# Kernel tuning notes

Measured on AMD Instinct MI355X. Metric: run time of the kernel, lower is better.

The kernel has to match this reference:

```python
import jax, jax.numpy as jnp
import numpy as np

EPS = float(np.finfo(float).eps)
NUM_RFS = 1

def conv3d(x, w):
    # x: [N,C,D,H,W], w: [O,I,kd,kh,kw], VALID, stride 1 (matches F.conv3d defaults)
    return jax.lax.conv_general_dilated(
        x, w, window_strides=(1, 1, 1), padding='VALID',
        dimension_numbers=('NCDHW', 'OIDHW', 'NCDHW'))

def setup_inputs() -> dict:
    key = jax.random.key(0)
    k1, k2, k3, k4 = jax.random.split(key, 4)
    x = jax.random.normal(k1, (1, 1, 3, 394, 394), jnp.float32)
    x_prev = jax.random.normal(k2, (1, 1, 3, 394, 394), jnp.float32)
    # params stored post-permute as [out_ch, in_ch, kt, kh, kw]
    filts_temp = jax.random.normal(k3, (16, 1, 3, 11, 11), jnp.float32)
    filts_notemp = jax.random.normal(k4, (16, 1, 1, 11, 11), jnp.float32)
    return {"x": x, "x_prev": x_prev, "filts_temp": filts_temp, "filts_notemp": filts_notemp}

def reference(x, x_prev, filts_temp, filts_notemp):
    corr_x = NUM_RFS * filts_temp.shape[3]  # kh
    corr_y = NUM_RFS * filts_temp.shape[4]  # kw
    num_filts = filts_temp.shape[0] + filts_notemp.shape[0]

    def feats(v):
        vt = jax.nn.relu(conv3d(v, filts_temp)) / 2           # [1,16,1,H',W'] (T==kt)
        vn = jax.nn.relu(conv3d(v[:, :, -1:, :, :], filts_notemp))  # last frame, [1,16,1,H',W']
        return jnp.concatenate([vt, vn], axis=1)              # [1,32,1,H',W']

    f = feats(x)
    fp = feats(x_prev)
    # channel-wise normalization
    x1 = f / (jnp.sum(f, axis=1, keepdims=True) + EPS)
    x1_prev = fp / (jnp.sum(fp, axis=1, keepdims=True) + EPS)

    y_max, x_max = x1.shape[3], x1.shape[4]
    yc = y_max - 2 * corr_y
    xc = x_max - 2 * corr_x
    # cropped current-frame channels become conv filters: [nf,1,1,yc,xc]
    x1_filts = x1[:, :, :, corr_y:y_max - corr_y, corr_x:x_max - corr_x].reshape(
        num_filts, 1, 1, yc, xc)
    prev = x1_prev.reshape(1, 1, num_filts, y_max, x_max)
    # normalized cross-correlation via conv3d: out [1, nf, nf, 2cy+1, 2cx+1]
    x2 = conv3d(prev, x1_filts)
    x2 = x2.reshape(1, num_filts, num_filts, 2 * corr_y + 1, 2 * corr_x + 1)
    x2 = x2 / ((y_max - 2 * corr_y) * (x_max - 2 * corr_y))  # faithful to original (uses corr_y twice)
    return x1, x2
```

## Files before the change

### kernel.cpp

```cpp
#include <hip/hip_runtime.h>
#include <hip/hip_bf16.h>


typedef unsigned short ushort_t;
typedef unsigned int uint_t;
typedef unsigned char uchar_t;
typedef __attribute__((ext_vector_type(4))) float f32x4;
typedef __attribute__((ext_vector_type(16))) float f32x16;
typedef __attribute__((ext_vector_type(4))) uint_t uint4_t;
typedef __attribute__((ext_vector_type(2))) uint_t uint2_t;

#define EPSF 2.2204460492503131e-16f
#define X1_N (32*384*384)
#define X2_N (32*32*23*23)

#define FILTB_BYTES (372*48*32*8)
#define PREVB_STRIDE 432
#define PREVB_BYTES (32*385*PREVB_STRIDE)
#define ZERO_BYTES ((size_t)FILTB_BYTES + PREVB_BYTES)
#define FT2_ELEMS (16*45*12)

#define YMAX 367
#define NCHUNKS 16
#define INV_AREA (1.0f/131044.0f)

#define SB_COPY_B 432
#define SB_DYB_B  (8*SB_COPY_B)
#define SB_ROW_B  (4*SB_DYB_B)

__device__ __forceinline__ uint_t f32_to_e4m3(float f) {
  if (f < 0.015625f)
    return (uint_t)__float2int_rn(f * 512.0f);
  uint_t b = __builtin_bit_cast(uint_t, f);
  int e = (int)(b >> 23) - 127;
  uint_t m = b & 0x7FFFFFu;
  uint_t keep = m >> 20;
  uint_t rest = m & 0xFFFFFu;
  keep += (rest > 0x80000u) || (rest == 0x80000u && (keep & 1u));
  if (keep == 8u) { keep = 0u; e += 1; }
  if (e > 8) return 0x7Eu;
  return (uint_t)(((e + 7) << 3) | keep);
}

__global__ void prep_kernel(const float* __restrict__ ft, const float* __restrict__ fn,
                            float* __restrict__ fT2)
{
  const int e = blockIdx.x * 256 + threadIdx.x;
  if (e < FT2_ELEMS) {
    const int chp = e / 540;
    const int rem = e - chp * 540;
    const int row = rem / 12;
    const int j = rem - row * 12;
    float v = 0.f;
    if (j < 11) {
      if (row < 33)      v = ft[chp * 363 + row * 11 + j];
      else if (row < 44) v = fn[chp * 121 + (row - 33) * 11 + j];
    }
    fT2[e] = v;
  }
}

__global__ __launch_bounds__(128, 4) void feat_kernel(
    const float* __restrict__ xcur, const float* __restrict__ xprev,
    const float* __restrict__ fT2,
    float* __restrict__ out_x1, uchar_t* __restrict__ prevb)
{
  __shared__ float sPx[3 * 18 * 28];
  const int tid = threadIdx.x;
  const int chp = tid & 15;
  const int r = tid >> 4;
  const int j0 = blockIdx.x * 16;
  const int i0 = blockIdx.y * 8;
  const int i = i0 + r;
  const int mode = blockIdx.z;
  const float* __restrict__ xin = mode ? xprev : xcur;

  for (int e = tid; e < 3 * 18 * 26; e += 128) {
    const int t = e / 468;
    const int rem = e - t * 468;
    const int ri = rem / 26;
    const int ci = rem - ri * 26;
    sPx[(t * 18 + ri) * 28 + ci] = xin[((size_t)t * 394 + i0 + ri) * 394 + j0 + ci];
  }
  __syncthreads();

  const float* __restrict__ fbase = fT2 + chp * 540;

  float accT[16], accN[16];
#pragma unroll
  for (int p = 0; p < 16; ++p) { accT[p] = 0.f; accN[p] = 0.f; }

#pragma unroll
  for (int t = 0; t < 3; ++t) {
    for (int a = 0; a < 11; ++a) {
      const float* row = &sPx[(t * 18 + r + a) * 28];
      float wv[26];
#pragma unroll
      for (int k = 0; k < 6; ++k) {
        const f32x4 q = *(const f32x4*)(row + 4 * k);
        wv[4 * k + 0] = q[0]; wv[4 * k + 1] = q[1];
        wv[4 * k + 2] = q[2]; wv[4 * k + 3] = q[3];
      }
      wv[24] = row[24]; wv[25] = row[25];

      const float* fr = fbase + (t * 11 + a) * 12;
      const f32x4 fq0 = *(const f32x4*)(fr);
      const f32x4 fq1 = *(const f32x4*)(fr + 4);
      const f32x4 fq2 = *(const f32x4*)(fr + 8);
      float fv[12];
#pragma unroll
      for (int k = 0; k < 4; ++k) { fv[k] = fq0[k]; fv[4+k] = fq1[k]; fv[8+k] = fq2[k]; }
      float fv2[12];
      if (t == 2) {
        const float* fr2 = fbase + (33 + a) * 12;
        const f32x4 g0 = *(const f32x4*)(fr2);
        const f32x4 g1 = *(const f32x4*)(fr2 + 4);
        const f32x4 g2 = *(const f32x4*)(fr2 + 8);
#pragma unroll
        for (int k = 0; k < 4; ++k) { fv2[k] = g0[k]; fv2[4+k] = g1[k]; fv2[8+k] = g2[k]; }
      }

#pragma unroll
      for (int b = 0; b < 11; ++b) {
        const float fT = fv[b];
#pragma unroll
        for (int p = 0; p < 16; ++p) accT[p] = fmaf(wv[b + p], fT, accT[p]);
        if (t == 2) {
          const float fN = fv2[b];
#pragma unroll
          for (int p = 0; p < 16; ++p) accN[p] = fmaf(wv[b + p], fN, accN[p]);
        }
      }
    }
  }

  float o0[16], o1[16];
#pragma unroll
  for (int p = 0; p < 16; ++p) {
    const float vT = fmaxf(accT[p], 0.f) * 0.5f;
    const float vN = fmaxf(accN[p], 0.f);
    float s = vT + vN;
    s += __shfl_xor(s, 1);  s += __shfl_xor(s, 2);
    s += __shfl_xor(s, 4);  s += __shfl_xor(s, 8);
    const float inv = 1.f / (s + EPSF);
    o0[p] = vT * inv;
    o1[p] = vN * inv;
  }

  if (mode == 0) {
#pragma unroll
    for (int q = 0; q < 4; ++q) {
      f32x4 v0 = {o0[4*q], o0[4*q+1], o0[4*q+2], o0[4*q+3]};
      f32x4 v1 = {o1[4*q], o1[4*q+1], o1[4*q+2], o1[4*q+3]};
      *(f32x4*)(out_x1 + (size_t)chp * 147456 + i * 384 + j0 + 4 * q) = v0;
      *(f32x4*)(out_x1 + (size_t)(chp + 16) * 147456 + i * 384 + j0 + 4 * q) = v1;
    }
  } else {
    uint4_t u0, u1;
#pragma unroll
    for (int q = 0; q < 4; ++q) {
      u0[q] = f32_to_e4m3(o0[4*q]) | (f32_to_e4m3(o0[4*q+1]) << 8) |
              (f32_to_e4m3(o0[4*q+2]) << 16) | (f32_to_e4m3(o0[4*q+3]) << 24);
      u1[q] = f32_to_e4m3(o1[4*q]) | (f32_to_e4m3(o1[4*q+1]) << 8) |
              (f32_to_e4m3(o1[4*q+2]) << 16) | (f32_to_e4m3(o1[4*q+3]) << 24);
    }
    *(uint4_t*)(prevb + ((size_t)chp * 385 + i) * PREVB_STRIDE + j0) = u0;
    *(uint4_t*)(prevb + ((size_t)(chp + 16) * 385 + i) * PREVB_STRIDE + j0) = u1;
  }
}

__global__ __launch_bounds__(256) void pack_kernel(
    const float* __restrict__ x1, uchar_t* __restrict__ filtb)
{
  const int e = blockIdx.x * 256 + threadIdx.x;
  if (e >= 362 * 46 * 32) return;
  const int o = e & 31;
  const int q = e >> 5;
  const int xb = q % 46;
  const int rowr = q / 46 + 5;
  const int i = rowr + 6;
  const int j0 = 11 + xb * 8;
  const float* src = x1 + (size_t)o * 147456 + i * 384 + j0;
  uint_t w0 = 0, w1 = 0;
#pragma unroll
  for (int k = 0; k < 4; ++k) {
    w0 |= f32_to_e4m3((j0 + k     <= 372) ? src[k]     : 0.f) << (8 * k);
    w1 |= f32_to_e4m3((j0 + 4 + k <= 372) ? src[4 + k] : 0.f) << (8 * k);
  }
  uint2_t u = {w0, w1};
  *(uint2_t*)(filtb + (((size_t)(rowr * 48 + xb) * 32 + o) << 3)) = u;
}

__global__ __launch_bounds__(768, 3) void corr_kernel(
    const uchar_t* __restrict__ filtb, const uchar_t* __restrict__ prevb,
    float* __restrict__ x2)
{
  __shared__ uint_t sB[2 * 2 * (SB_ROW_B / 4)];

  const int tid = threadIdx.x;
  const int lane = tid & 63;
  const int wv = tid >> 6;
  const int cg = (wv >= 6) ? 1 : 0;
  const int w = wv - 6 * cg;
  const int kg = lane >> 5;
  const int nn = lane & 31;

  const int chpair = blockIdx.x / NCHUNKS;
  const int chunk = blockIdx.x % NCHUNKS;
  const int ch = 2 * chpair + cg;
  const int y0 = (chunk * YMAX) / NCHUNKS;
  const int y1 = ((chunk + 1) * YMAX) / NCHUNKS;

  uint_t* const sBg = sB + cg * (2 * (SB_ROW_B / 4));

  int boffB[3];
#pragma unroll
  for (int nt = 0; nt < 3; ++nt) {
    const int n = nt * 32 + nn;
    const int dyb = n / 24;
    const int dxr = n - 24 * dyb;
    const int dx = (dxr < 23) ? dxr : 22;
    const int s = dx & 7;
    boffB[nt] = dyb * SB_DYB_B + s * SB_COPY_B + (dx >> 3) * 8 + kg * 8;
  }

  const int tl = tid - cg * 384;
  const bool st_act = (tl < 104);
  const int sdyb = st_act ? (tl / 26) : 0;
  const int sg = tl - 26 * (st_act ? (tl / 26) : 0);
  const uchar_t* srcbase = prevb + ((size_t)(ch * 385 + 6 * sdyb)) * PREVB_STRIDE;
  const int dstoff = sdyb * (SB_DYB_B / 4) + 4 * sg;

  uint_t st0 = 0, st1 = 0, st2 = 0, st3 = 0, st4 = 0, st5 = 0;

  auto load_st = [&](int yy) {
    const uint_t* sw = (const uint_t*)(srcbase + (size_t)yy * PREVB_STRIDE) + 4 * sg;
    const uint4_t lo = *(const uint4_t*)(sw);
    const uint2_t hi = *(const uint2_t*)(sw + 4);
    st0 = lo.x; st1 = lo.y; st2 = lo.z; st3 = lo.w; st4 = hi.x; st5 = hi.y;
  };

  auto write_shift = [&](int buf) {
    uint_t* dst = sBg + buf * (SB_ROW_B / 4) + dstoff;
    const uint_t wd[6] = {st0, st1, st2, st3, st4, st5};
#pragma unroll
    for (int s = 0; s < 8; ++s) {
      const int off = s >> 2;
      const int b = (s & 3) * 8;
      uint4_t v;
      if (b == 0) {
        v = uint4_t{wd[off], wd[off + 1], wd[off + 2], wd[off + 3]};
      } else {
        v = uint4_t{(wd[off]     >> b) | (wd[off + 1] << (32 - b)),
                    (wd[off + 1] >> b) | (wd[off + 2] << (32 - b)),
                    (wd[off + 2] >> b) | (wd[off + 3] << (32 - b)),
                    (wd[off + 3] >> b) | (wd[off + 4] << (32 - b))};
      }
      *(uint4_t*)(dst + s * (SB_COPY_B / 4)) = v;
    }
  };

  f32x16 acc[3];
#pragma unroll
  for (int nt = 0; nt < 3; ++nt)
#pragma unroll
    for (int r = 0; r < 16; ++r) acc[nt][r] = 0.f;

  if (st_act) {
    load_st(y0);
    write_shift(0);
    if (y0 + 1 < y1) load_st(y0 + 1);
  }

  const uchar_t* aptr = filtb + (size_t)(y0 - w + 5) * 12288 + kg * 256 + nn * 8;
  long Af0 = *(const long*)(aptr);
  long Af1 = *(const long*)(aptr + 512);

  __syncthreads();

  for (int y = y0; y < y1; ++y) {
    const int pb = (y - y0) & 1;

    if (st_act && y + 1 < y1) write_shift(pb ^ 1);
    if (st_act && y + 2 < y1) load_st(y + 2);

    const char* sBrd = (const char*)sBg + pb * SB_ROW_B;

    long Af2, Bf[3], Bfn[3];
#pragma unroll
    for (int nt = 0; nt < 3; ++nt)
      Bf[nt] = *(const long*)(sBrd + boffB[nt]);

#pragma unroll
    for (int Kt = 0; Kt < 24; ++Kt) {
      Af2 = *(const long*)(aptr + ((Kt + 2) << 9));
      const int Ktb = (Kt + 1 < 24) ? Kt + 1 : 23;
#pragma unroll
      for (int nt = 0; nt < 3; ++nt)
        Bfn[nt] = *(const long*)(sBrd + boffB[nt] + (Ktb << 4));
#pragma unroll
      for (int nt = 0; nt < 3; ++nt)
        acc[nt] = __builtin_amdgcn_mfma_f32_32x32x16_fp8_fp8(
            Af0, Bf[nt], acc[nt], 0, 0, 0);
      Af0 = Af1; Af1 = Af2;
#pragma unroll
      for (int nt = 0; nt < 3; ++nt) Bf[nt] = Bfn[nt];
    }
    aptr += 12288;

    __syncthreads();
  }

#pragma unroll
  for (int nt = 0; nt < 3; ++nt) {
    const int n = nt * 32 + nn;
    const int dyb = n / 24;
    const int dxr = n - 24 * dyb;
    if (dxr < 23) {
      const int dy = w + 6 * dyb;
      if (dy <= 22) {
#pragma unroll
        for (int r = 0; r < 16; ++r) {
          const int o = (r & 3) + 8 * (r >> 2) + 4 * kg;
          atomicAdd(&x2[((o * 32 + ch) * 23 + dy) * 23 + dxr],
                    acc[nt][r] * INV_AREA);
        }
      }
    }
  }
}

extern "C" void kernel_launch(void* const* d_in, const int* in_sizes, int n_in,
                              void* d_out, int out_size, void* d_ws, size_t ws_size,
                              hipStream_t stream)
{
  const float* x     = (const float*)d_in[0];
  const float* xprev = (const float*)d_in[1];
  const float* ft    = (const float*)d_in[2];
  const float* fn    = (const float*)d_in[3];
  float* out = (float*)d_out;

  uchar_t* filtb = (uchar_t*)d_ws;
  uchar_t* prevb = filtb + FILTB_BYTES;
  float* fT2 = (float*)(prevb + PREVB_BYTES);

  hipMemsetAsync(d_ws, 0, ZERO_BYTES, stream);
  hipMemsetAsync(out + X1_N, 0, (size_t)X2_N * sizeof(float), stream);

  prep_kernel<<<dim3((FT2_ELEMS + 255) / 256), 256, 0, stream>>>(ft, fn, fT2);
  feat_kernel<<<dim3(24, 48, 2), 128, 0, stream>>>(x, xprev, fT2, out, prevb);
  pack_kernel<<<dim3((362 * 46 * 32 + 255) / 256), 256, 0, stream>>>(out, filtb);
  corr_kernel<<<dim3(16 * NCHUNKS), 768, 0, stream>>>(filtb, prevb, out + X1_N);
}
```

Baseline: 303.4 us.

## Stage filter rows through an LDS ring buffer in the correlation kernel

The correlation kernel now keeps the fp8 filter (A operand) rows in an 8-row LDS ring buffer instead of reading them directly from global memory in the inner MFMA loop. Each block loads one new row per iteration with a 16-byte-per-thread cooperative load, then stores it to LDS after the MFMA loop. The 12 waves share that row instead of each re-fetching its own global loads. The cost is about 98 KB more shared memory through dynamic allocation, which may reduce occupancy. A-fragment reads also become LDS reads that compete with the B-operand LDS traffic.

New measurement: 293.7 us. -3.2%, faster.

```diff
diff --git a/kernel.cpp b/kernel.cpp
--- a/kernel.cpp
+++ b/kernel.cpp
@@ -14,6 +14,7 @@
 #define X1_N (32*384*384)
 #define X2_N (32*32*23*23)
 
+#define FILTB_ROW_B 12288
 #define FILTB_BYTES (372*48*32*8)
 #define PREVB_STRIDE 432
 #define PREVB_BYTES (32*385*PREVB_STRIDE)
@@ -27,6 +28,10 @@
 #define SB_COPY_B 432
 #define SB_DYB_B  (8*SB_COPY_B)
 #define SB_ROW_B  (4*SB_DYB_B)
+#define SB_BYTES  (2*2*SB_ROW_B)
+
+#define SA_BYTES  (8*FILTB_ROW_B)
+#define SMEM_TOTAL (SA_BYTES + SB_BYTES)
 
 __device__ __forceinline__ uint_t f32_to_e4m3(float f) {
   if (f < 0.015625f)
@@ -195,7 +200,7 @@
     const uchar_t* __restrict__ filtb, const uchar_t* __restrict__ prevb,
     float* __restrict__ x2)
 {
-  __shared__ uint_t sB[2 * 2 * (SB_ROW_B / 4)];
+  extern __shared__ uchar_t smem[];
 
   const int tid = threadIdx.x;
   const int lane = tid & 63;
@@ -211,7 +216,7 @@
   const int y0 = (chunk * YMAX) / NCHUNKS;
   const int y1 = ((chunk + 1) * YMAX) / NCHUNKS;
 
-  uint_t* const sBg = sB + cg * (2 * (SB_ROW_B / 4));
+  uint_t* const sBg = (uint_t*)(smem + SA_BYTES) + cg * (2 * (SB_ROW_B / 4));
 
   int boffB[3];
 #pragma unroll
@@ -266,47 +271,62 @@
 #pragma unroll
     for (int r = 0; r < 16; ++r) acc[nt][r] = 0.f;
 
+  {
+    uint4_t pv[6];
+#pragma unroll
+    for (int r6 = 0; r6 < 6; ++r6)
+      pv[r6] = *(const uint4_t*)(filtb + (size_t)(y0 + r6) * FILTB_ROW_B + tid * 16);
+#pragma unroll
+    for (int r6 = 0; r6 < 6; ++r6)
+      *(uint4_t*)(smem + ((y0 + r6) & 7) * FILTB_ROW_B + tid * 16) = pv[r6];
+  }
   if (st_act) {
     load_st(y0);
     write_shift(0);
     if (y0 + 1 < y1) load_st(y0 + 1);
   }
 
-  const uchar_t* aptr = filtb + (size_t)(y0 - w + 5) * 12288 + kg * 256 + nn * 8;
-  long Af0 = *(const long*)(aptr);
-  long Af1 = *(const long*)(aptr + 512);
-
   __syncthreads();
 
   for (int y = y0; y < y1; ++y) {
     const int pb = (y - y0) & 1;
 
+    const bool a_act = (y + 6 <= y1 + 4);
+    uint4_t aval;
+    if (a_act)
+      aval = *(const uint4_t*)(filtb + (size_t)(y + 6) * FILTB_ROW_B + tid * 16);
+
     if (st_act && y + 1 < y1) write_shift(pb ^ 1);
     if (st_act && y + 2 < y1) load_st(y + 2);
 
     const char* sBrd = (const char*)sBg + pb * SB_ROW_B;
-
-    long Af2, Bf[3], Bfn[3];
+    const char* aRow = (const char*)smem +
+        ((y + 5 - w) & 7) * FILTB_ROW_B + kg * 256 + nn * 8;
+
+    long Af, Afn, Bf[3], Bfn[3];
+    Af = *(const long*)(aRow);
 #pragma unroll
     for (int nt = 0; nt < 3; ++nt)
       Bf[nt] = *(const long*)(sBrd + boffB[nt]);
 
 #pragma unroll
     for (int Kt = 0; Kt < 24; ++Kt) {
-      Af2 = *(const long*)(aptr + ((Kt + 2) << 9));
-      const int Ktb = (Kt + 1 < 24) ? Kt + 1 : 23;
+      const int Ktn = (Kt + 1 < 24) ? Kt + 1 : 23;
+      Afn = *(const long*)(aRow + (Ktn << 9));
 #pragma unroll
       for (int nt = 0; nt < 3; ++nt)
-        Bfn[nt] = *(const long*)(sBrd + boffB[nt] + (Ktb << 4));
+        Bfn[nt] = *(const long*)(sBrd + boffB[nt] + (Ktn << 4));
 #pragma unroll
       for (int nt = 0; nt < 3; ++nt)
         acc[nt] = __builtin_amdgcn_mfma_f32_32x32x16_fp8_fp8(
-            Af0, Bf[nt], acc[nt], 0, 0, 0);
-      Af0 = Af1; Af1 = Af2;
+            Af, Bf[nt], acc[nt], 0, 0, 0);
+      Af = Afn;
 #pragma unroll
       for (int nt = 0; nt < 3; ++nt) Bf[nt] = Bfn[nt];
     }
-    aptr += 12288;
+
+    if (a_act)
+      *(uint4_t*)(smem + ((y + 6) & 7) * FILTB_ROW_B + tid * 16) = aval;
 
     __syncthreads();
   }
@@ -344,11 +364,19 @@
   uchar_t* prevb = filtb + FILTB_BYTES;
   float* fT2 = (float*)(prevb + PREVB_BYTES);
 
+  static bool attr_set = false;
+  if (!attr_set) {
+    (void)hipFuncSetAttribute((const void*)corr_kernel,
+        hipFuncAttributeMaxDynamicSharedMemorySize, SMEM_TOTAL);
+    attr_set = true;
+  }
+
   hipMemsetAsync(d_ws, 0, ZERO_BYTES, stream);
   hipMemsetAsync(out + X1_N, 0, (size_t)X2_N * sizeof(float), stream);
 
   prep_kernel<<<dim3((FT2_ELEMS + 255) / 256), 256, 0, stream>>>(ft, fn, fT2);
   feat_kernel<<<dim3(24, 48, 2), 128, 0, stream>>>(x, xprev, fT2, out, prevb);
   pack_kernel<<<dim3((362 * 46 * 32 + 255) / 256), 256, 0, stream>>>(out, filtb);
-  corr_kernel<<<dim3(16 * NCHUNKS), 768, 0, stream>>>(filtb, prevb, out + X1_N);
-}
+  corr_kernel<<<dim3(16 * NCHUNKS), 768, SMEM_TOTAL, stream>>>(
+      filtb, prevb, out + X1_N);
+}
```
